# Kernel optimization log

Hardware: AMD Instinct MI355X
Metric: run time of the kernel (lower is better)

The kernel has to match this reference:

```python
import jax, jax.numpy as jnp
import numpy as np

B, RES, DIM, H, KD = 16, 32, 768, 12, 64
N = RES * RES          # 1024 tokens
D = KD                 # attn_ratio = 1 -> per-head value dim == key_dim
DH = D * H             # 768
SCALE = KD ** -0.5
LN_EPS = 1e-5


def _bias_idxs():
    # replicate the itertools.product construction: for row-major points,
    # offsets (|dy|,|dx|) are first seen in order dy-major, so id = |dy|*RES + |dx|
    coords = np.arange(N)
    y, x = coords // RES, coords % RES
    dy = np.abs(y[:, None] - y[None, :])
    dx = np.abs(x[:, None] - x[None, :])
    return jnp.asarray(dy * RES + dx, dtype=jnp.int32)  # [N, N]


def setup_inputs() -> dict:
    key = jax.random.key(0)
    ks = jax.random.split(key, 8)
    return {
        "x": jax.random.normal(ks[0], (B, N, DIM), jnp.float32),
        "ln_w": 1.0 + 0.01 * jax.random.normal(ks[1], (DIM,), jnp.float32),
        "ln_b": 0.01 * jax.random.normal(ks[2], (DIM,), jnp.float32),
        "qkv_w": 0.02 * jax.random.normal(ks[3], (3 * H * KD, DIM), jnp.float32),
        "qkv_b": 0.01 * jax.random.normal(ks[4], (3 * H * KD,), jnp.float32),
        "proj_w": 0.02 * jax.random.normal(ks[5], (DIM, DH), jnp.float32),
        "proj_b": 0.01 * jax.random.normal(ks[6], (DIM,), jnp.float32),
        "attn_biases": 0.1 * jax.random.normal(ks[7], (H, RES * RES), jnp.float32),
        "bias_idxs": _bias_idxs(),
    }


def reference(x, ln_w, ln_b, qkv_w, qkv_b, proj_w, proj_b, attn_biases, bias_idxs):
    # LayerNorm over the feature dim
    mu = jnp.mean(x, axis=-1, keepdims=True)
    var = jnp.mean(jnp.square(x - mu), axis=-1, keepdims=True)
    xn = (x - mu) * jax.lax.rsqrt(var + LN_EPS) * ln_w + ln_b

    # fused qkv projection -> [B, N, H, 3*KD], split per head
    qkv = (xn @ qkv_w.T + qkv_b).reshape(B, N, H, 3 * KD)
    q, k, v = jnp.split(qkv, [KD, 2 * KD], axis=3)  # each [B, N, H, KD]

    # gathered relative-position bias: [H, N, N]
    bias = attn_biases[:, bias_idxs]

    # scores + bias -> softmax -> AV
    attn = jnp.einsum("bnhk,bmhk->bhnm", q, k) * SCALE + bias[None]
    attn = jax.nn.softmax(attn, axis=-1)
    out = jnp.einsum("bhnm,bmhd->bnhd", attn, v).reshape(B, N, DH)
    return out @ proj_w.T + proj_b
```

## Files before the change

kernel.cpp:

```cpp
#include <hip/hip_runtime.h>
#include <cstdint>
#include <cstddef>

#define AS1 __attribute__((address_space(1)))
#define AS3 __attribute__((address_space(3)))

typedef float f32x4 __attribute__((ext_vector_type(4)));
typedef __bf16 bf16x8 __attribute__((ext_vector_type(8)));
typedef __bf16 bf16x4 __attribute__((ext_vector_type(4)));
typedef uint32_t u32x4 __attribute__((ext_vector_type(4)));

__device__ __forceinline__ void async_cp16(void* lds, const void* g) {
    __builtin_amdgcn_global_load_lds((AS1 void*)(g), (AS3 void*)(lds), 16, 0, 0);
}

__device__ __forceinline__ bf16x8 frag_of(u32x4 u) {
    return __builtin_bit_cast(bf16x8, u);
}

__global__ __launch_bounds__(256) void cvt_bf16(const float* __restrict__ in,
                                                __bf16* __restrict__ out, int n4) {
    int i = blockIdx.x * 256 + threadIdx.x;
    if (i < n4) {
        float4 v = ((const float4*)in)[i];
        bf16x4 o;
        o.x = (__bf16)v.x; o.y = (__bf16)v.y; o.z = (__bf16)v.z; o.w = (__bf16)v.w;
        ((bf16x4*)out)[i] = o;
    }
}

__global__ __launch_bounds__(256)
void ln_kernel(const float* __restrict__ x, const float* __restrict__ w,
               const float* __restrict__ bsh, __bf16* __restrict__ xn) {
    const int lane = threadIdx.x & 63;
    const long row = (long)blockIdx.x * 4 + (threadIdx.x >> 6);
    const float4* xr = (const float4*)(x + row * 768);
    float4 v[3];
    v[0] = xr[lane]; v[1] = xr[lane + 64]; v[2] = xr[lane + 128];
    float s = 0.f, ss = 0.f;
#pragma unroll
    for (int i = 0; i < 3; ++i) {
        s  += v[i].x + v[i].y + v[i].z + v[i].w;
        ss += v[i].x * v[i].x + v[i].y * v[i].y + v[i].z * v[i].z + v[i].w * v[i].w;
    }
#pragma unroll
    for (int m = 1; m < 64; m <<= 1) { s += __shfl_xor(s, m); ss += __shfl_xor(ss, m); }
    const float mean = s * (1.f / 768.f);
    const float rstd = rsqrtf(ss * (1.f / 768.f) - mean * mean + 1e-5f);
    const float4* wv = (const float4*)w;
    const float4* bv = (const float4*)bsh;
    bf16x4* outp = (bf16x4*)(xn + row * 768);
#pragma unroll
    for (int i = 0; i < 3; ++i) {
        float4 wi = wv[lane + 64 * i], bi = bv[lane + 64 * i];
        bf16x4 o;
        o.x = (__bf16)((v[i].x - mean) * rstd * wi.x + bi.x);
        o.y = (__bf16)((v[i].y - mean) * rstd * wi.y + bi.y);
        o.z = (__bf16)((v[i].z - mean) * rstd * wi.z + bi.z);
        o.w = (__bf16)((v[i].w - mean) * rstd * wi.w + bi.w);
        outp[lane + 64 * i] = o;
    }
}

template <int MODE>
__global__ __launch_bounds__(256, 2)
void gemm_nt(const __bf16* __restrict__ A, const __bf16* __restrict__ Bw,
             const float* __restrict__ bias,
             __bf16* __restrict__ q_out, __bf16* __restrict__ k_out,
             __bf16* __restrict__ v_out, float* __restrict__ f_out) {
    constexpr int K = 768;
    __shared__ __align__(16) __bf16 As[128 * 32];
    __shared__ __align__(16) __bf16 Bs[128 * 32];
    const int tid  = threadIdx.x;
    const int lane = tid & 63;
    const int quad = lane >> 4;
    const int l16  = lane & 15;
    const int wave = tid >> 6;
    const int wm = wave >> 1, wn = wave & 1;
    const long bm = (long)blockIdx.y * 128;
    const long bn = (long)blockIdx.x * 128;

    const __bf16* Ab = A  + bm * K;
    const __bf16* Bb = Bw + bn * K;

    const int el0 = tid;
    const int el1 = tid + 256;
    const int rA0 = el0 >> 2, rA1 = el1 >> 2;
    const int kc  = (tid & 3) * 8;

    f32x4 acc[4][4] = {};

    for (int k0 = 0; k0 < K; k0 += 32) {
        __syncthreads();
        async_cp16((char*)As + el0 * 16, Ab + (long)rA0 * K + (k0 + kc));
        async_cp16((char*)As + el1 * 16, Ab + (long)rA1 * K + (k0 + kc));
        async_cp16((char*)Bs + el0 * 16, Bb + (long)rA0 * K + (k0 + kc));
        async_cp16((char*)Bs + el1 * 16, Bb + (long)rA1 * K + (k0 + kc));
        __syncthreads();

        const u32x4* Av = (const u32x4*)As;
        const u32x4* Bv = (const u32x4*)Bs;
        bf16x8 af[4], bfr[4];
#pragma unroll
        for (int t = 0; t < 4; ++t) {
            af[t]  = frag_of(Av[(wm * 64 + t * 16 + l16) * 4 + quad]);
            bfr[t] = frag_of(Bv[(wn * 64 + t * 16 + l16) * 4 + quad]);
        }
#pragma unroll
        for (int i = 0; i < 4; ++i)
#pragma unroll
            for (int j = 0; j < 4; ++j) {
                if constexpr (MODE == 0)
                    acc[i][j] = __builtin_amdgcn_mfma_f32_16x16x32_bf16(bfr[j], af[i], acc[i][j], 0, 0, 0);
                else
                    acc[i][j] = __builtin_amdgcn_mfma_f32_16x16x32_bf16(af[i], bfr[j], acc[i][j], 0, 0, 0);
            }
    }

    if constexpr (MODE == 0) {
        float4 bb[4];
#pragma unroll
        for (int j = 0; j < 4; ++j)
            bb[j] = *(const float4*)(bias + (int)bn + wn * 64 + j * 16 + quad * 4);
#pragma unroll
        for (int i = 0; i < 4; ++i) {
            long row = bm + wm * 64 + i * 16 + l16;
            long b   = row >> 10;
            long n   = row & 1023;
#pragma unroll
            for (int j = 0; j < 4; ++j) {
                int col0 = (int)bn + wn * 64 + j * 16 + quad * 4;
                int h  = col0 / 192;
                int rr = col0 - h * 192;
                int t  = rr >> 6;
                int d  = rr & 63;
                bf16x4 pk;
                pk[0] = (__bf16)(acc[i][j][0] + bb[j].x);
                pk[1] = (__bf16)(acc[i][j][1] + bb[j].y);
                pk[2] = (__bf16)(acc[i][j][2] + bb[j].z);
                pk[3] = (__bf16)(acc[i][j][3] + bb[j].w);
                __bf16* dst = (t == 0) ? q_out : ((t == 1) ? k_out : v_out);
                *(bf16x4*)(dst + ((b * 12 + h) * 1024 + n) * 64 + d) = pk;
            }
        }
    } else {
#pragma unroll
        for (int i = 0; i < 4; ++i) {
#pragma unroll
            for (int r = 0; r < 4; ++r) {
                long row = bm + wm * 64 + i * 16 + quad * 4 + r;
#pragma unroll
                for (int j = 0; j < 4; ++j) {
                    int col = (int)bn + wn * 64 + j * 16 + l16;
                    f_out[row * 768 + col] = acc[i][j][r] + bias[col];
                }
            }
        }
    }
}

__global__ __launch_bounds__(256)
void vtrans(const __bf16* __restrict__ V, __bf16* __restrict__ Vt) {
    __shared__ __align__(16) __bf16 T[64 * 64];
    const int tid = threadIdx.x;
    const int nt = blockIdx.x, h = blockIdx.y, b = blockIdx.z;
    const long bh = (long)b * 12 + h;
    const __bf16* Vg = V + (bh * 1024 + nt * 64) * 64;
    const int e0 = tid, e1 = tid + 256;
    const int r0 = e0 >> 3, c0 = (e0 & 7) ^ (r0 & 7);
    const int r1 = e1 >> 3, c1 = (e1 & 7) ^ (r1 & 7);
    async_cp16((char*)T + e0 * 16, Vg + r0 * 64 + c0 * 8);
    async_cp16((char*)T + e1 * 16, Vg + r1 * 64 + c1 * 8);
    __syncthreads();
    __bf16* Vo = Vt + bh * 64 * 1024 + nt * 64;
#pragma unroll
    for (int p = 0; p < 2; ++p) {
        int dr = p * 32 + (tid >> 3);
        int nc = tid & 7;
        bf16x8 o;
#pragma unroll
        for (int u = 0; u < 8; ++u) {
            int rr = nc * 8 + u;
            o[u] = T[rr * 64 + (((dr >> 3) ^ (rr & 7)) << 3) + (dr & 7)];
        }
        *(bf16x8*)(Vo + (long)dr * 1024 + nc * 8) = o;
    }
}

__global__ __launch_bounds__(256, 4)
void attn_kernel(const __bf16* __restrict__ Q, const __bf16* __restrict__ Kb,
                 const __bf16* __restrict__ Vt, const float* __restrict__ biases,
                 __bf16* __restrict__ out) {
    __shared__ __align__(16) __bf16 QPs[64 * 64];
    __shared__ __align__(16) __bf16 Ks[64 * 64];
    __shared__ __align__(16) __bf16 Vts[64 * 64];
    __shared__ __align__(16) float brow[1024];

    const int tid  = threadIdx.x;
    const int lane = tid & 63;
    const int wave = tid >> 6;
    const int quad = lane >> 4;
    const int l16  = lane & 15;
    const int sw   = l16 & 7;
    const int qt = blockIdx.x;
    const int h  = blockIdx.y;
    const int b  = blockIdx.z;

    const long bh = (long)b * 12 + h;
    const __bf16* Qg  = Q  + (bh * 1024 + qt * 64) * 64;
    const __bf16* Kg  = Kb + bh * 1024 * 64;
    const __bf16* Vtg = Vt + bh * 64 * 1024;

    const int e0 = tid, e1 = tid + 256;
    const int r0 = e0 >> 3, c0 = (e0 & 7) ^ (r0 & 7);
    const int r1 = e1 >> 3, c1 = (e1 & 7) ^ (r1 & 7);

    async_cp16((char*)QPs + e0 * 16, Qg + r0 * 64 + c0 * 8);
    async_cp16((char*)QPs + e1 * 16, Qg + r1 * 64 + c1 * 8);
    {
        const float LOG2E = 1.4426950408889634f;
        float4 v = ((const float4*)(biases + (long)h * 1024))[tid];
        float4 o; o.x = v.x * LOG2E; o.y = v.y * LOG2E; o.z = v.z * LOG2E; o.w = v.w * LOG2E;
        ((float4*)brow)[tid] = o;
    }
    __syncthreads();

    bf16x8 aq[2];
    {
        const u32x4* Qv = (const u32x4*)QPs;
        int qrow = wave * 16 + l16;
        aq[0] = frag_of(Qv[qrow * 8 + (quad ^ sw)]);
        aq[1] = frag_of(Qv[qrow * 8 + ((quad + 4) ^ sw)]);
    }

    const int yq = 2 * qt + (wave >> 1);
    const int xq = ((wave & 1) << 4) + l16;
    int pdx[2][4];
#pragma unroll
    for (int i2 = 0; i2 < 2; ++i2)
#pragma unroll
        for (int r = 0; r < 4; ++r) {
            int xk = (i2 << 4) + quad * 4 + r;
            int d = xq - xk; pdx[i2][r] = d < 0 ? -d : d;
        }

    const float SSCALE = 0.125f * 1.4426950408889634f;
    float lacc = 0.f;
    f32x4 o[4] = {};
    __bf16* Psw = QPs + wave * 1024;
    const int pwb = l16 * 128 + (quad & 1) * 8;

    for (int kt = 0; kt < 16; ++kt) {
        __syncthreads();
        {
            const __bf16* Kt  = Kg + kt * 4096;
            const __bf16* Vtt = Vtg + kt * 64;
            async_cp16((char*)Ks + e0 * 16, Kt + r0 * 64 + c0 * 8);
            async_cp16((char*)Ks + e1 * 16, Kt + r1 * 64 + c1 * 8);
            async_cp16((char*)Vts + e0 * 16, Vtt + r0 * 1024 + c0 * 8);
            async_cp16((char*)Vts + e1 * 16, Vtt + r1 * 1024 + c1 * 8);
        }
        __syncthreads();

        f32x4 s[4];
        const u32x4* Kv = (const u32x4*)Ks;
#pragma unroll
        for (int nt = 0; nt < 4; ++nt) {
            int krow = nt * 16 + l16;
            bf16x8 k0 = frag_of(Kv[krow * 8 + (quad ^ sw)]);
            bf16x8 k1 = frag_of(Kv[krow * 8 + ((quad + 4) ^ sw)]);
            f32x4 z = {0.f, 0.f, 0.f, 0.f};
            z = __builtin_amdgcn_mfma_f32_16x16x32_bf16(k0, aq[0], z, 0, 0, 0);
            z = __builtin_amdgcn_mfma_f32_16x16x32_bf16(k1, aq[1], z, 0, 0, 0);
            s[nt] = z;
        }

        int dy0 = yq - 2 * kt;     dy0 = dy0 < 0 ? -dy0 : dy0;
        int dy1 = yq - 2 * kt - 1; dy1 = dy1 < 0 ? -dy1 : dy1;
        const float* br0 = brow + dy0 * 32;
        const float* br1 = brow + dy1 * 32;
#pragma unroll
        for (int nt = 0; nt < 4; ++nt) {
            const float* br = (nt & 2) ? br1 : br0;
            bf16x4 pk;
#pragma unroll
            for (int r = 0; r < 4; ++r) {
                float p = __builtin_amdgcn_exp2f(s[nt][r] * SSCALE + br[pdx[nt & 1][r]]);
                lacc += p;
                pk[r] = (__bf16)p;
            }
            *(bf16x4*)((char*)Psw + pwb + (((nt * 2 + (quad >> 1)) ^ sw) << 4)) = pk;
        }

        const u32x4* Pv = (const u32x4*)Psw;
        const u32x4* Vv = (const u32x4*)Vts;
        bf16x8 bp0 = frag_of(Pv[l16 * 8 + (quad ^ sw)]);
        bf16x8 bp1 = frag_of(Pv[l16 * 8 + ((quad + 4) ^ sw)]);
#pragma unroll
        for (int dt = 0; dt < 4; ++dt) {
            int vrow = dt * 16 + l16;
            bf16x8 v0 = frag_of(Vv[vrow * 8 + (quad ^ sw)]);
            bf16x8 v1 = frag_of(Vv[vrow * 8 + ((quad + 4) ^ sw)]);
            o[dt] = __builtin_amdgcn_mfma_f32_16x16x32_bf16(v0, bp0, o[dt], 0, 0, 0);
            o[dt] = __builtin_amdgcn_mfma_f32_16x16x32_bf16(v1, bp1, o[dt], 0, 0, 0);
        }
    }

    lacc += __shfl_xor(lacc, 16);
    lacc += __shfl_xor(lacc, 32);
    const float rl = 1.f / lacc;

    const long n = qt * 64 + wave * 16 + l16;
    __bf16* op = out + ((long)b * 1024 + n) * 768 + h * 64 + quad * 4;
#pragma unroll
    for (int dt = 0; dt < 4; ++dt) {
        bf16x4 ov;
        ov[0] = (__bf16)(o[dt][0] * rl);
        ov[1] = (__bf16)(o[dt][1] * rl);
        ov[2] = (__bf16)(o[dt][2] * rl);
        ov[3] = (__bf16)(o[dt][3] * rl);
        *(bf16x4*)(op + dt * 16) = ov;
    }
}

extern "C" void kernel_launch(void* const* d_in, const int* in_sizes, int n_in,
                              void* d_out, int out_size, void* d_ws, size_t ws_size,
                              hipStream_t stream) {
    (void)in_sizes; (void)n_in; (void)out_size; (void)ws_size;
    const float* x      = (const float*)d_in[0];
    const float* ln_w   = (const float*)d_in[1];
    const float* ln_b   = (const float*)d_in[2];
    const float* qkv_w  = (const float*)d_in[3];
    const float* qkv_b  = (const float*)d_in[4];
    const float* proj_w = (const float*)d_in[5];
    const float* proj_b = (const float*)d_in[6];
    const float* ab     = (const float*)d_in[7];
    float* outp = (float*)d_out;

    char* ws = (char*)d_ws;
    __bf16* xn     = (__bf16*)(ws);
    __bf16* vtb    = (__bf16*)(ws);
    __bf16* qkvwb  = (__bf16*)(ws + 25165824);
    __bf16* projwb = (__bf16*)(ws + 28704768);
    __bf16* qb     = (__bf16*)(ws + 29884416);
    __bf16* kb     = (__bf16*)(ws + 55050240);
    __bf16* vb     = (__bf16*)(ws + 80216064);
    __bf16* aout   = (__bf16*)(ws + 80216064);

    cvt_bf16<<<1728, 256, 0, stream>>>(qkv_w, qkvwb, 442368);
    cvt_bf16<<<576, 256, 0, stream>>>(proj_w, projwb, 147456);
    ln_kernel<<<4096, 256, 0, stream>>>(x, ln_w, ln_b, xn);
    gemm_nt<0><<<dim3(18, 128), 256, 0, stream>>>(xn, qkvwb, qkv_b, qb, kb, vb, nullptr);
    vtrans<<<dim3(16, 12, 16), 256, 0, stream>>>(vb, vtb);
    attn_kernel<<<dim3(16, 12, 16), 256, 0, stream>>>(qb, kb, vtb, ab, aout);
    gemm_nt<1><<<dim3(6, 128), 256, 0, stream>>>(aout, projwb, proj_b, nullptr, nullptr, nullptr, outp);
}
```

Baseline: 335.2 us.

## Fuse V transpose into QKV GEMM epilogue and double query tile per attention block

Weight conversion is merged into one kernel that also reorders qkv_w rows so Q, K and V columns are contiguous. The QKV GEMM then writes V directly in transposed layout from MODE 2 blocks, which removes the separate vtrans kernel and its extra round trip through memory. The attention kernel now processes 128 queries per block (32 per wave), reusing each loaded K/V tile across two query groups and halving the grid. This raises register and LDS pressure per block, and the transposed V stores are narrower and less coalesced.

```diff
diff --git a/kernel.cpp b/kernel.cpp
--- a/kernel.cpp
+++ b/kernel.cpp
@@ -18,14 +18,26 @@
     return __builtin_bit_cast(bf16x8, u);
 }
 
-__global__ __launch_bounds__(256) void cvt_bf16(const float* __restrict__ in,
-                                                __bf16* __restrict__ out, int n4) {
+__global__ __launch_bounds__(256)
+void cvt_w(const float* __restrict__ qkvw, const float* __restrict__ projw,
+           __bf16* __restrict__ qkvwb, __bf16* __restrict__ projwb) {
     int i = blockIdx.x * 256 + threadIdx.x;
-    if (i < n4) {
-        float4 v = ((const float4*)in)[i];
+    if (i < 442368) {
+        int row = i / 192, c4 = (i - row * 192) * 4;
+        int t = (row >= 1536) ? 2 : (row >= 768 ? 1 : 0);
+        int rem = row - t * 768;
+        int hh = rem >> 6, d = rem & 63;
+        int in_row = hh * 192 + t * 64 + d;
+        float4 v = *(const float4*)(qkvw + (long)in_row * 768 + c4);
         bf16x4 o;
-        o.x = (__bf16)v.x; o.y = (__bf16)v.y; o.z = (__bf16)v.z; o.w = (__bf16)v.w;
-        ((bf16x4*)out)[i] = o;
+        o[0] = (__bf16)v.x; o[1] = (__bf16)v.y; o[2] = (__bf16)v.z; o[3] = (__bf16)v.w;
+        *(bf16x4*)(qkvwb + (long)row * 768 + c4) = o;
+    } else {
+        int j = i - 442368;
+        float4 v = ((const float4*)projw)[j];
+        bf16x4 o;
+        o[0] = (__bf16)v.x; o[1] = (__bf16)v.y; o[2] = (__bf16)v.z; o[3] = (__bf16)v.w;
+        ((bf16x4*)projwb)[j] = o;
     }
 }
 
@@ -54,37 +66,34 @@
     for (int i = 0; i < 3; ++i) {
         float4 wi = wv[lane + 64 * i], bi = bv[lane + 64 * i];
         bf16x4 o;
-        o.x = (__bf16)((v[i].x - mean) * rstd * wi.x + bi.x);
-        o.y = (__bf16)((v[i].y - mean) * rstd * wi.y + bi.y);
-        o.z = (__bf16)((v[i].z - mean) * rstd * wi.z + bi.z);
-        o.w = (__bf16)((v[i].w - mean) * rstd * wi.w + bi.w);
+        o[0] = (__bf16)((v[i].x - mean) * rstd * wi.x + bi.x);
+        o[1] = (__bf16)((v[i].y - mean) * rstd * wi.y + bi.y);
+        o[2] = (__bf16)((v[i].z - mean) * rstd * wi.z + bi.z);
+        o[3] = (__bf16)((v[i].w - mean) * rstd * wi.w + bi.w);
         outp[lane + 64 * i] = o;
     }
 }
 
 template <int MODE>
-__global__ __launch_bounds__(256, 2)
-void gemm_nt(const __bf16* __restrict__ A, const __bf16* __restrict__ Bw,
-             const float* __restrict__ bias,
-             __bf16* __restrict__ q_out, __bf16* __restrict__ k_out,
-             __bf16* __restrict__ v_out, float* __restrict__ f_out) {
+__device__ __forceinline__
+void gemm_core(__bf16* As, __bf16* Bs,
+               const __bf16* __restrict__ A, const __bf16* __restrict__ Bw,
+               const float* __restrict__ bias,
+               __bf16* __restrict__ q_out, __bf16* __restrict__ k_out,
+               __bf16* __restrict__ vt_out, float* __restrict__ f_out,
+               long bm, long bn) {
     constexpr int K = 768;
-    __shared__ __align__(16) __bf16 As[128 * 32];
-    __shared__ __align__(16) __bf16 Bs[128 * 32];
     const int tid  = threadIdx.x;
     const int lane = tid & 63;
     const int quad = lane >> 4;
     const int l16  = lane & 15;
     const int wave = tid >> 6;
     const int wm = wave >> 1, wn = wave & 1;
-    const long bm = (long)blockIdx.y * 128;
-    const long bn = (long)blockIdx.x * 128;
 
     const __bf16* Ab = A  + bm * K;
     const __bf16* Bb = Bw + bn * K;
 
-    const int el0 = tid;
-    const int el1 = tid + 256;
+    const int el0 = tid, el1 = tid + 256;
     const int rA0 = el0 >> 2, rA1 = el1 >> 2;
     const int kc  = (tid & 3) * 8;
 
@@ -118,29 +127,45 @@
     }
 
     if constexpr (MODE == 0) {
-        float4 bb[4];
-#pragma unroll
-        for (int j = 0; j < 4; ++j)
-            bb[j] = *(const float4*)(bias + (int)bn + wn * 64 + j * 16 + quad * 4);
-#pragma unroll
-        for (int i = 0; i < 4; ++i) {
-            long row = bm + wm * 64 + i * 16 + l16;
-            long b   = row >> 10;
-            long n   = row & 1023;
-#pragma unroll
-            for (int j = 0; j < 4; ++j) {
-                int col0 = (int)bn + wn * 64 + j * 16 + quad * 4;
-                int h  = col0 / 192;
-                int rr = col0 - h * 192;
-                int t  = rr >> 6;
-                int d  = rr & 63;
+#pragma unroll
+        for (int j = 0; j < 4; ++j) {
+            int col0 = (int)bn + wn * 64 + j * 16 + quad * 4;
+            int t  = col0 >= 768;
+            int cc = col0 - t * 768;
+            int h  = cc >> 6, d = cc & 63;
+            int f  = h * 192 + t * 64 + d;
+            float4 bb = *(const float4*)(bias + f);
+            __bf16* dst = t ? k_out : q_out;
+#pragma unroll
+            for (int i = 0; i < 4; ++i) {
+                long row = bm + wm * 64 + i * 16 + l16;
+                long b   = row >> 10;
+                long n   = row & 1023;
                 bf16x4 pk;
-                pk[0] = (__bf16)(acc[i][j][0] + bb[j].x);
-                pk[1] = (__bf16)(acc[i][j][1] + bb[j].y);
-                pk[2] = (__bf16)(acc[i][j][2] + bb[j].z);
-                pk[3] = (__bf16)(acc[i][j][3] + bb[j].w);
-                __bf16* dst = (t == 0) ? q_out : ((t == 1) ? k_out : v_out);
+                pk[0] = (__bf16)(acc[i][j][0] + bb.x);
+                pk[1] = (__bf16)(acc[i][j][1] + bb.y);
+                pk[2] = (__bf16)(acc[i][j][2] + bb.z);
+                pk[3] = (__bf16)(acc[i][j][3] + bb.w);
                 *(bf16x4*)(dst + ((b * 12 + h) * 1024 + n) * 64 + d) = pk;
+            }
+        }
+    } else if constexpr (MODE == 2) {
+#pragma unroll
+        for (int j = 0; j < 4; ++j) {
+            int cv = (int)bn - 1536 + wn * 64 + j * 16 + l16;
+            int h  = cv >> 6, d = cv & 63;
+            float bv = bias[h * 192 + 128 + d];
+#pragma unroll
+            for (int i = 0; i < 4; ++i) {
+                long row0 = bm + wm * 64 + i * 16 + quad * 4;
+                long b    = row0 >> 10;
+                long n0   = row0 & 1023;
+                bf16x4 pk;
+                pk[0] = (__bf16)(acc[i][j][0] + bv);
+                pk[1] = (__bf16)(acc[i][j][1] + bv);
+                pk[2] = (__bf16)(acc[i][j][2] + bv);
+                pk[3] = (__bf16)(acc[i][j][3] + bv);
+                *(bf16x4*)(vt_out + ((b * 12 + h) * 64 + d) * 1024 + n0) = pk;
             }
         }
     } else {
@@ -159,39 +184,35 @@
     }
 }
 
-__global__ __launch_bounds__(256)
-void vtrans(const __bf16* __restrict__ V, __bf16* __restrict__ Vt) {
-    __shared__ __align__(16) __bf16 T[64 * 64];
-    const int tid = threadIdx.x;
-    const int nt = blockIdx.x, h = blockIdx.y, b = blockIdx.z;
-    const long bh = (long)b * 12 + h;
-    const __bf16* Vg = V + (bh * 1024 + nt * 64) * 64;
-    const int e0 = tid, e1 = tid + 256;
-    const int r0 = e0 >> 3, c0 = (e0 & 7) ^ (r0 & 7);
-    const int r1 = e1 >> 3, c1 = (e1 & 7) ^ (r1 & 7);
-    async_cp16((char*)T + e0 * 16, Vg + r0 * 64 + c0 * 8);
-    async_cp16((char*)T + e1 * 16, Vg + r1 * 64 + c1 * 8);
-    __syncthreads();
-    __bf16* Vo = Vt + bh * 64 * 1024 + nt * 64;
-#pragma unroll
-    for (int p = 0; p < 2; ++p) {
-        int dr = p * 32 + (tid >> 3);
-        int nc = tid & 7;
-        bf16x8 o;
-#pragma unroll
-        for (int u = 0; u < 8; ++u) {
-            int rr = nc * 8 + u;
-            o[u] = T[rr * 64 + (((dr >> 3) ^ (rr & 7)) << 3) + (dr & 7)];
-        }
-        *(bf16x8*)(Vo + (long)dr * 1024 + nc * 8) = o;
-    }
+__global__ __launch_bounds__(256, 2)
+void gemm_qkv(const __bf16* __restrict__ A, const __bf16* __restrict__ Bw,
+              const float* __restrict__ bias, __bf16* __restrict__ qb,
+              __bf16* __restrict__ kb, __bf16* __restrict__ vtb) {
+    __shared__ __align__(16) __bf16 As[128 * 32];
+    __shared__ __align__(16) __bf16 Bs[128 * 32];
+    int blk = blockIdx.x;
+    int bx = blk % 18;
+    long by = blk / 18;
+    if (bx < 12)
+        gemm_core<0>(As, Bs, A, Bw, bias, qb, kb, nullptr, nullptr, by * 128, (long)bx * 128);
+    else
+        gemm_core<2>(As, Bs, A, Bw, bias, nullptr, nullptr, vtb, nullptr, by * 128, (long)bx * 128);
+}
+
+__global__ __launch_bounds__(256, 2)
+void gemm_proj(const __bf16* __restrict__ A, const __bf16* __restrict__ Bw,
+               const float* __restrict__ bias, float* __restrict__ out) {
+    __shared__ __align__(16) __bf16 As[128 * 32];
+    __shared__ __align__(16) __bf16 Bs[128 * 32];
+    gemm_core<1>(As, Bs, A, Bw, bias, nullptr, nullptr, nullptr, out,
+                 (long)blockIdx.y * 128, (long)blockIdx.x * 128);
 }
 
 __global__ __launch_bounds__(256, 4)
 void attn_kernel(const __bf16* __restrict__ Q, const __bf16* __restrict__ Kb,
                  const __bf16* __restrict__ Vt, const float* __restrict__ biases,
                  __bf16* __restrict__ out) {
-    __shared__ __align__(16) __bf16 QPs[64 * 64];
+    __shared__ __align__(16) __bf16 QPs[128 * 64];
     __shared__ __align__(16) __bf16 Ks[64 * 64];
     __shared__ __align__(16) __bf16 Vts[64 * 64];
     __shared__ __align__(16) float brow[1024];
@@ -207,16 +228,15 @@
     const int b  = blockIdx.z;
 
     const long bh = (long)b * 12 + h;
-    const __bf16* Qg  = Q  + (bh * 1024 + qt * 64) * 64;
+    const __bf16* Qg  = Q  + (bh * 1024 + qt * 128) * 64;
     const __bf16* Kg  = Kb + bh * 1024 * 64;
     const __bf16* Vtg = Vt + bh * 64 * 1024;
 
-    const int e0 = tid, e1 = tid + 256;
-    const int r0 = e0 >> 3, c0 = (e0 & 7) ^ (r0 & 7);
-    const int r1 = e1 >> 3, c1 = (e1 & 7) ^ (r1 & 7);
-
-    async_cp16((char*)QPs + e0 * 16, Qg + r0 * 64 + c0 * 8);
-    async_cp16((char*)QPs + e1 * 16, Qg + r1 * 64 + c1 * 8);
+#pragma unroll
+    for (int p = 0; p < 4; ++p) {
+        int e = tid + p * 256, r = e >> 3, c = (e & 7) ^ (r & 7);
+        async_cp16((char*)QPs + e * 16, Qg + r * 64 + c * 8);
+    }
     {
         const float LOG2E = 1.4426950408889634f;
         float4 v = ((const float4*)(biases + (long)h * 1024))[tid];
@@ -225,30 +245,37 @@
     }
     __syncthreads();
 
-    bf16x8 aq[2];
+    bf16x8 aq[2][2];
     {
         const u32x4* Qv = (const u32x4*)QPs;
-        int qrow = wave * 16 + l16;
-        aq[0] = frag_of(Qv[qrow * 8 + (quad ^ sw)]);
-        aq[1] = frag_of(Qv[qrow * 8 + ((quad + 4) ^ sw)]);
-    }
-
-    const int yq = 2 * qt + (wave >> 1);
-    const int xq = ((wave & 1) << 4) + l16;
-    int pdx[2][4];
-#pragma unroll
-    for (int i2 = 0; i2 < 2; ++i2)
-#pragma unroll
-        for (int r = 0; r < 4; ++r) {
-            int xk = (i2 << 4) + quad * 4 + r;
-            int d = xq - xk; pdx[i2][r] = d < 0 ? -d : d;
-        }
+#pragma unroll
+        for (int g = 0; g < 2; ++g) {
+            int qrow = wave * 32 + g * 16 + l16;
+            aq[g][0] = frag_of(Qv[qrow * 8 + (quad ^ sw)]);
+            aq[g][1] = frag_of(Qv[qrow * 8 + ((quad + 4) ^ sw)]);
+        }
+    }
+
+    const int yq = qt * 4 + wave;
+    int pdxb[2][2][4];
+#pragma unroll
+    for (int g = 0; g < 2; ++g)
+#pragma unroll
+        for (int i2 = 0; i2 < 2; ++i2)
+#pragma unroll
+            for (int r = 0; r < 4; ++r) {
+                int d = (g * 16 + l16) - (i2 * 16 + quad * 4 + r);
+                pdxb[g][i2][r] = (d < 0 ? -d : d) * 4;
+            }
 
     const float SSCALE = 0.125f * 1.4426950408889634f;
-    float lacc = 0.f;
-    f32x4 o[4] = {};
-    __bf16* Psw = QPs + wave * 1024;
-    const int pwb = l16 * 128 + (quad & 1) * 8;
+    float lacc[2] = {0.f, 0.f};
+    f32x4 o[2][4] = {};
+    __bf16* Psw = QPs + wave * 2048;
+
+    const int e0 = tid, e1 = tid + 256;
+    const int r0 = e0 >> 3, c0 = (e0 & 7) ^ (r0 & 7);
+    const int r1 = e1 >> 3, c1 = (e1 & 7) ^ (r1 & 7);
 
     for (int kt = 0; kt < 16; ++kt) {
         __syncthreads();
@@ -262,64 +289,83 @@
         }
         __syncthreads();
 
-        f32x4 s[4];
+        f32x4 s[2][4];
         const u32x4* Kv = (const u32x4*)Ks;
 #pragma unroll
         for (int nt = 0; nt < 4; ++nt) {
             int krow = nt * 16 + l16;
             bf16x8 k0 = frag_of(Kv[krow * 8 + (quad ^ sw)]);
             bf16x8 k1 = frag_of(Kv[krow * 8 + ((quad + 4) ^ sw)]);
-            f32x4 z = {0.f, 0.f, 0.f, 0.f};
-            z = __builtin_amdgcn_mfma_f32_16x16x32_bf16(k0, aq[0], z, 0, 0, 0);
-            z = __builtin_amdgcn_mfma_f32_16x16x32_bf16(k1, aq[1], z, 0, 0, 0);
-            s[nt] = z;
+#pragma unroll
+            for (int g = 0; g < 2; ++g) {
+                f32x4 z = {0.f, 0.f, 0.f, 0.f};
+                z = __builtin_amdgcn_mfma_f32_16x16x32_bf16(k0, aq[g][0], z, 0, 0, 0);
+                z = __builtin_amdgcn_mfma_f32_16x16x32_bf16(k1, aq[g][1], z, 0, 0, 0);
+                s[g][nt] = z;
+            }
         }
 
         int dy0 = yq - 2 * kt;     dy0 = dy0 < 0 ? -dy0 : dy0;
         int dy1 = yq - 2 * kt - 1; dy1 = dy1 < 0 ? -dy1 : dy1;
-        const float* br0 = brow + dy0 * 32;
-        const float* br1 = brow + dy1 * 32;
-#pragma unroll
-        for (int nt = 0; nt < 4; ++nt) {
-            const float* br = (nt & 2) ? br1 : br0;
-            bf16x4 pk;
-#pragma unroll
-            for (int r = 0; r < 4; ++r) {
-                float p = __builtin_amdgcn_exp2f(s[nt][r] * SSCALE + br[pdx[nt & 1][r]]);
-                lacc += p;
-                pk[r] = (__bf16)p;
-            }
-            *(bf16x4*)((char*)Psw + pwb + (((nt * 2 + (quad >> 1)) ^ sw) << 4)) = pk;
+        const char* br0 = (const char*)(brow + dy0 * 32);
+        const char* br1 = (const char*)(brow + dy1 * 32);
+#pragma unroll
+        for (int g = 0; g < 2; ++g) {
+            int rowb = (g * 16 + l16) * 128 + (quad & 1) * 8;
+#pragma unroll
+            for (int nt = 0; nt < 4; ++nt) {
+                const char* br = (nt & 2) ? br1 : br0;
+                bf16x4 pk;
+#pragma unroll
+                for (int r = 0; r < 4; ++r) {
+                    float bvv = *(const float*)(br + pdxb[g][nt & 1][r]);
+                    float p = __builtin_amdgcn_exp2f(s[g][nt][r] * SSCALE + bvv);
+                    lacc[g] += p;
+                    pk[r] = (__bf16)p;
+                }
+                *(bf16x4*)((char*)Psw + rowb + (((nt * 2 + (quad >> 1)) ^ sw) << 4)) = pk;
+            }
         }
 
         const u32x4* Pv = (const u32x4*)Psw;
         const u32x4* Vv = (const u32x4*)Vts;
-        bf16x8 bp0 = frag_of(Pv[l16 * 8 + (quad ^ sw)]);
-        bf16x8 bp1 = frag_of(Pv[l16 * 8 + ((quad + 4) ^ sw)]);
+        bf16x8 bp[2][2];
+#pragma unroll
+        for (int g = 0; g < 2; ++g) {
+            int prow = g * 16 + l16;
+            bp[g][0] = frag_of(Pv[prow * 8 + (quad ^ sw)]);
+            bp[g][1] = frag_of(Pv[prow * 8 + ((quad + 4) ^ sw)]);
+        }
 #pragma unroll
         for (int dt = 0; dt < 4; ++dt) {
             int vrow = dt * 16 + l16;
             bf16x8 v0 = frag_of(Vv[vrow * 8 + (quad ^ sw)]);
             bf16x8 v1 = frag_of(Vv[vrow * 8 + ((quad + 4) ^ sw)]);
-            o[dt] = __builtin_amdgcn_mfma_f32_16x16x32_bf16(v0, bp0, o[dt], 0, 0, 0);
-            o[dt] = __builtin_amdgcn_mfma_f32_16x16x32_bf16(v1, bp1, o[dt], 0, 0, 0);
-        }
-    }
-
-    lacc += __shfl_xor(lacc, 16);
-    lacc += __shfl_xor(lacc, 32);
-    const float rl = 1.f / lacc;
-
-    const long n = qt * 64 + wave * 16 + l16;
-    __bf16* op = out + ((long)b * 1024 + n) * 768 + h * 64 + quad * 4;
-#pragma unroll
-    for (int dt = 0; dt < 4; ++dt) {
-        bf16x4 ov;
-        ov[0] = (__bf16)(o[dt][0] * rl);
-        ov[1] = (__bf16)(o[dt][1] * rl);
-        ov[2] = (__bf16)(o[dt][2] * rl);
-        ov[3] = (__bf16)(o[dt][3] * rl);
-        *(bf16x4*)(op + dt * 16) = ov;
+#pragma unroll
+            for (int g = 0; g < 2; ++g) {
+                o[g][dt] = __builtin_amdgcn_mfma_f32_16x16x32_bf16(v0, bp[g][0], o[g][dt], 0, 0, 0);
+                o[g][dt] = __builtin_amdgcn_mfma_f32_16x16x32_bf16(v1, bp[g][1], o[g][dt], 0, 0, 0);
+            }
+        }
+    }
+
+#pragma unroll
+    for (int g = 0; g < 2; ++g) {
+        float l = lacc[g];
+        l += __shfl_xor(l, 16);
+        l += __shfl_xor(l, 32);
+        const float rl = 1.f / l;
+        const long n = qt * 128 + wave * 32 + g * 16 + l16;
+        __bf16* op = out + ((long)b * 1024 + n) * 768 + h * 64 + quad * 4;
+#pragma unroll
+        for (int dt = 0; dt < 4; ++dt) {
+            bf16x4 ov;
+            ov[0] = (__bf16)(o[g][dt][0] * rl);
+            ov[1] = (__bf16)(o[g][dt][1] * rl);
+            ov[2] = (__bf16)(o[g][dt][2] * rl);
+            ov[3] = (__bf16)(o[g][dt][3] * rl);
+            *(bf16x4*)(op + dt * 16) = ov;
+        }
     }
 }
 
@@ -339,19 +385,16 @@
 
     char* ws = (char*)d_ws;
     __bf16* xn     = (__bf16*)(ws);
-    __bf16* vtb    = (__bf16*)(ws);
+    __bf16* aout   = (__bf16*)(ws);
     __bf16* qkvwb  = (__bf16*)(ws + 25165824);
     __bf16* projwb = (__bf16*)(ws + 28704768);
     __bf16* qb     = (__bf16*)(ws + 29884416);
     __bf16* kb     = (__bf16*)(ws + 55050240);
-    __bf16* vb     = (__bf16*)(ws + 80216064);
-    __bf16* aout   = (__bf16*)(ws + 80216064);
-
-    cvt_bf16<<<1728, 256, 0, stream>>>(qkv_w, qkvwb, 442368);
-    cvt_bf16<<<576, 256, 0, stream>>>(proj_w, projwb, 147456);
+    __bf16* vtb    = (__bf16*)(ws + 80216064);
+
+    cvt_w<<<2304, 256, 0, stream>>>(qkv_w, proj_w, qkvwb, projwb);
     ln_kernel<<<4096, 256, 0, stream>>>(x, ln_w, ln_b, xn);
-    gemm_nt<0><<<dim3(18, 128), 256, 0, stream>>>(xn, qkvwb, qkv_b, qb, kb, vb, nullptr);
-    vtrans<<<dim3(16, 12, 16), 256, 0, stream>>>(vb, vtb);
-    attn_kernel<<<dim3(16, 12, 16), 256, 0, stream>>>(qb, kb, vtb, ab, aout);
-    gemm_nt<1><<<dim3(6, 128), 256, 0, stream>>>(aout, projwb, proj_b, nullptr, nullptr, nullptr, outp);
-}
+    gemm_qkv<<<2304, 256, 0, stream>>>(xn, qkvwb, qkv_b, qb, kb, vtb);
+    attn_kernel<<<dim3(8, 12, 16), 256, 0, stream>>>(qb, kb, vtb, ab, aout);
+    gemm_proj<<<dim3(6, 128), 256, 0, stream>>>(aout, projwb, proj_b, outp);
+}
```

Result: slower. 348.3 us (+3.9%).
